# Performance work log

Hardware: AMD Instinct MI355X
Metric: run time of the kernel (lower is better)

## Reference

```python
import jax, jax.numpy as jnp
import numpy as np

B, N, IN_DIM, OUT_DIM = 8, 2048, 128, 128
NEG_SLOPE = 0.2

def setup_inputs() -> dict:
    key = jax.random.key(0)
    k1, k2, k3, k4 = jax.random.split(key, 4)
    x = jax.random.normal(k1, (B, N, IN_DIM), dtype=jnp.float32)
    adj = jax.random.randint(k2, (N, N), 0, 2, dtype=jnp.int32)
    # nn.Linear weight init scale ~ 1/sqrt(fan_in)
    W = jax.random.normal(k3, (IN_DIM, OUT_DIM), dtype=jnp.float32) / np.sqrt(IN_DIM)
    a_vec = jax.random.normal(k4, (2 * OUT_DIM,), dtype=jnp.float32) / np.sqrt(2 * OUT_DIM)
    return {"x": x, "adj": adj, "W": W, "a_vec": a_vec}

def reference(x, adj, W, a_vec):
    # h = x @ W : [b, n, d]
    h = jnp.einsum("bni,io->bno", x, W)
    # Algebraic decomposition of a([h_i, h_j]) = a1.h_i + a2.h_j
    a1, a2 = a_vec[:OUT_DIM], a_vec[OUT_DIM:]
    s_i = h @ a1  # [b, n] score contribution from source node i
    s_j = h @ a2  # [b, n] score contribution from target node j
    e = s_i[:, :, None] + s_j[:, None, :]  # [b, n, n]
    e = jnp.where(e >= 0, e, NEG_SLOPE * e)  # leaky_relu(0.2)
    mask = (adj > 0)[None, :, :]  # [1, n, n] broadcast over batch
    e = jnp.where(mask, e, -jnp.inf)
    alpha = jax.nn.softmax(e, axis=-1)  # [b, n, n]
    out = jnp.einsum("bnm,bmd->bnd", alpha, h)  # [b, n, d]
    return out, alpha
```

## Files before the change

### kernel.cpp

```cpp
#include <hip/hip_runtime.h>
#include <hip/hip_bf16.h>
#include <cstdint>
#include <cstddef>

constexpr int Bn = 8;
constexpr int Nn = 2048;
constexpr int Dn = 128;

typedef __bf16 bf16x8 __attribute__((ext_vector_type(8)));
typedef float f32x4 __attribute__((ext_vector_type(4)));

#define AS1 __attribute__((address_space(1)))
#define AS3 __attribute__((address_space(3)))

static __device__ __forceinline__ void gl_lds16(const void* g, void* l) {
  __builtin_amdgcn_global_load_lds((AS1 const void*)g, (AS3 void*)l, 16, 0, 0);
}

__global__ __launch_bounds__(256) void gat_k0(
    const int* __restrict__ adj, unsigned long long* __restrict__ mask64) {
  const int t = threadIdx.x;
  const size_t g = (size_t)blockIdx.x * 256 + t;
  int v = adj[g];
  unsigned long long bal = __ballot(v > 0);
  if ((t & 63) == 0) mask64[g >> 6] = bal;
}

__global__ __launch_bounds__(256) void gat_k1(
    const float* __restrict__ x, const float* __restrict__ W,
    const float* __restrict__ a_vec,
    __bf16* __restrict__ hT, float* __restrict__ s1, float* __restrict__ s2) {
  __shared__ __align__(16) float Wl[64 * 144];
  __shared__ __align__(16) float xL[32 * 132];

  const int t = threadIdx.x;
  const int r0 = blockIdx.x * 32;
  const int b = r0 >> 11;
  const int n0 = r0 & (Nn - 1);
  const int rp = (t >> 4) << 1;
  const int c0 = (t & 15) << 3;
  const int c0p = c0 + ((c0 >> 5) << 2);

  float acc[2][8];
#pragma unroll
  for (int r = 0; r < 2; ++r)
#pragma unroll
    for (int c = 0; c < 8; ++c) acc[r][c] = 0.f;

#pragma unroll
  for (int it = 0; it < 4; ++it) {
    int idx = t + (it << 8);
    int rr = idx >> 5, kc = (idx & 31) << 2;
    *(float4*)(xL + rr * 132 + kc) = *(const float4*)(x + (size_t)(r0 + rr) * Dn + kc);
  }

  for (int ph = 0; ph < 2; ++ph) {
    if (ph) __syncthreads();
#pragma unroll
    for (int it = 0; it < 8; ++it) {
      int idx = t + (it << 8);
      int kk = idx >> 5, c4 = (idx & 31) << 2;
      int dsto = kk * 144 + c4 + ((c4 >> 5) << 2);
      *(float4*)(Wl + dsto) = *(const float4*)(W + (size_t)((ph << 6) + kk) * Dn + c4);
    }
    __syncthreads();
    const float* xrow = xL + rp * 132 + (ph << 6);
    for (int k = 0; k < 64; ++k) {
      float xa0 = xrow[k];
      float xa1 = xrow[132 + k];
      float4 w0 = *(const float4*)(Wl + k * 144 + c0p);
      float4 w1 = *(const float4*)(Wl + k * 144 + c0p + 4);
      float ws[8] = {w0.x, w0.y, w0.z, w0.w, w1.x, w1.y, w1.z, w1.w};
#pragma unroll
      for (int c = 0; c < 8; ++c) {
        acc[0][c] = fmaf(xa0, ws[c], acc[0][c]);
        acc[1][c] = fmaf(xa1, ws[c], acc[1][c]);
      }
    }
  }

  float q1[2] = {0.f, 0.f}, q2[2] = {0.f, 0.f};
#pragma unroll
  for (int c = 0; c < 8; ++c) {
    float a1c = a_vec[c0 + c];
    float a2c = a_vec[Dn + c0 + c];
    q1[0] = fmaf(acc[0][c], a1c, q1[0]);
    q1[1] = fmaf(acc[1][c], a1c, q1[1]);
    q2[0] = fmaf(acc[0][c], a2c, q2[0]);
    q2[1] = fmaf(acc[1][c], a2c, q2[1]);
  }
#pragma unroll
  for (int d = 1; d < 16; d <<= 1) {
    q1[0] += __shfl_xor(q1[0], d);
    q1[1] += __shfl_xor(q1[1], d);
    q2[0] += __shfl_xor(q2[0], d);
    q2[1] += __shfl_xor(q2[1], d);
  }
  if ((t & 15) == 0) {
    s1[b * Nn + n0 + rp] = q1[0];
    s1[b * Nn + n0 + rp + 1] = q1[1];
    s2[b * Nn + n0 + rp] = q2[0];
    s2[b * Nn + n0 + rp + 1] = q2[1];
  }

#pragma unroll
  for (int c = 0; c < 8; ++c) {
    union { __bf16 h[2]; uint32_t u; } pk;
    pk.h[0] = (__bf16)acc[0][c];
    pk.h[1] = (__bf16)acc[1][c];
    *(uint32_t*)(hT + (size_t)(b * Dn + c0 + c) * Nn + n0 + rp) = pk.u;
  }
}

__global__ __launch_bounds__(512) void gat_k2(
    const uint32_t* __restrict__ mask, const __bf16* __restrict__ hT,
    const float* __restrict__ s1, const float* __restrict__ s2,
    float* __restrict__ out, float* __restrict__ alpha) {
  __shared__ __align__(16) float sj[Nn];
  __shared__ float siv[32], invl[32];
  __shared__ __align__(16) __bf16 Pl[2][32 * 72];
  __shared__ __align__(16) __bf16 hl[2][128 * 64];

  const int t = threadIdx.x;
  const int b = blockIdx.x & 7;
  const int i0 = (blockIdx.x >> 3) << 5;
  const int w = t >> 6, lane = t & 63;
  const int ii = t >> 4, sub = t & 15;
  const int lrow = lane >> 3, ccs = lane & 7;
  const __bf16* __restrict__ hTb = hT + (size_t)b * Dn * Nn;

#pragma unroll
  for (int inst = 0; inst < 2; ++inst) {
    int row = (w << 4) + (inst << 3) + lrow;
    gl_lds16(hTb + (size_t)row * Nn + ((ccs ^ lrow) << 3),
             &hl[0][((w << 4) + (inst << 3)) << 6]);
  }

  *(float4*)(sj + (t << 2)) = *(const float4*)(s2 + b * Nn + (t << 2));
  if (t < 32) siv[t] = s1[b * Nn + i0 + t];
  __syncthreads();

  const int i = i0 + ii;
  const uint32_t* __restrict__ mrow = mask + ((size_t)i << 6);
  const float si = siv[ii];

  float l = 0.f;
  const int wofs = sub >> 3;
  const int bsh = (sub & 7) << 2;
  for (int cc = 0; cc < 32; ++cc) {
    int j = (cc << 6) + (sub << 2);
    uint32_t mw = mrow[(cc << 1) + wofs];
    float4 sv = *(const float4*)(sj + j);
    float e;
    e = si + sv.x; e = fmaxf(e, 0.2f * e); l += ((mw >> (bsh + 0)) & 1u) ? __expf(e) : 0.f;
    e = si + sv.y; e = fmaxf(e, 0.2f * e); l += ((mw >> (bsh + 1)) & 1u) ? __expf(e) : 0.f;
    e = si + sv.z; e = fmaxf(e, 0.2f * e); l += ((mw >> (bsh + 2)) & 1u) ? __expf(e) : 0.f;
    e = si + sv.w; e = fmaxf(e, 0.2f * e); l += ((mw >> (bsh + 3)) & 1u) ? __expf(e) : 0.f;
  }
  l += __shfl_xor(l, 1);
  l += __shfl_xor(l, 2);
  l += __shfl_xor(l, 4);
  l += __shfl_xor(l, 8);
  if (sub == 0) invl[ii] = 1.f / l;
  __syncthreads();
  const float il = invl[ii];

  const int iw = (w & 1) << 4;
  const int nd0 = (w >> 1) << 5;
  const int q16 = lane >> 4, m16 = lane & 15;
  f32x4 acc0 = {0.f, 0.f, 0.f, 0.f}, acc1 = {0.f, 0.f, 0.f, 0.f};
  float* __restrict__ arow = alpha + ((size_t)(b * Nn + i) << 11);

  for (int jt = 0; jt < 32; ++jt) {
    const int buf = jt & 1;
    const int j0 = jt << 6;
    {
      int j = j0 + (sub << 2);
      uint32_t mw = mrow[(j0 >> 5) + wofs];
      float4 sv = *(const float4*)(sj + j);
      float e0 = si + sv.x; e0 = fmaxf(e0, 0.2f * e0);
      float e1 = si + sv.y; e1 = fmaxf(e1, 0.2f * e1);
      float e2 = si + sv.z; e2 = fmaxf(e2, 0.2f * e2);
      float e3 = si + sv.w; e3 = fmaxf(e3, 0.2f * e3);
      float a0 = ((mw >> (bsh + 0)) & 1u) ? __expf(e0) * il : 0.f;
      float a1 = ((mw >> (bsh + 1)) & 1u) ? __expf(e1) * il : 0.f;
      float a2 = ((mw >> (bsh + 2)) & 1u) ? __expf(e2) * il : 0.f;
      float a3 = ((mw >> (bsh + 3)) & 1u) ? __expf(e3) * il : 0.f;
      *(float4*)(arow + j) = make_float4(a0, a1, a2, a3);
      union { __bf16 h[4]; uint2 u; } pk;
      pk.h[0] = (__bf16)a0; pk.h[1] = (__bf16)a1;
      pk.h[2] = (__bf16)a2; pk.h[3] = (__bf16)a3;
      *(uint2*)(&Pl[buf][ii * 72 + (sub << 2)]) = pk.u;
    }
    __syncthreads();
    if (jt < 31) {
      int jn = j0 + 64;
#pragma unroll
      for (int inst = 0; inst < 2; ++inst) {
        int row = (w << 4) + (inst << 3) + lrow;
        gl_lds16(hTb + (size_t)row * Nn + jn + ((ccs ^ lrow) << 3),
                 &hl[buf ^ 1][((w << 4) + (inst << 3)) << 6]);
      }
    }
#pragma unroll
    for (int ks = 0; ks < 2; ++ks) {
      bf16x8 af = *(const bf16x8*)(&Pl[buf][(iw + m16) * 72 + (ks << 5) + (q16 << 3)]);
      {
        int d = nd0 + m16;
        int phys = ((ks << 2) + q16) ^ (d & 7);
        bf16x8 bv = *(const bf16x8*)(&hl[buf][(d << 6) + (phys << 3)]);
        acc0 = __builtin_amdgcn_mfma_f32_16x16x32_bf16(af, bv, acc0, 0, 0, 0);
      }
      {
        int d = nd0 + 16 + m16;
        int phys = ((ks << 2) + q16) ^ (d & 7);
        bf16x8 bv = *(const bf16x8*)(&hl[buf][(d << 6) + (phys << 3)]);
        acc1 = __builtin_amdgcn_mfma_f32_16x16x32_bf16(af, bv, acc1, 0, 0, 0);
      }
    }
  }

#pragma unroll
  for (int nb = 0; nb < 2; ++nb) {
    f32x4 a = nb ? acc1 : acc0;
    int d = nd0 + (nb << 4) + m16;
#pragma unroll
    for (int r = 0; r < 4; ++r) {
      int irow = i0 + iw + (q16 << 2) + r;
      out[((size_t)(b * Nn + irow) << 7) + d] = a[r];
    }
  }
}

extern "C" void kernel_launch(void* const* d_in, const int* in_sizes, int n_in,
                              void* d_out, int out_size, void* d_ws, size_t ws_size,
                              hipStream_t stream) {
  const float* x = (const float*)d_in[0];
  const int* adj = (const int*)d_in[1];
  const float* W = (const float*)d_in[2];
  const float* a_vec = (const float*)d_in[3];

  float* out = (float*)d_out;
  float* alpha = out + (size_t)Bn * Nn * Dn;

  char* ws = (char*)d_ws;
  __bf16* hT = (__bf16*)ws;
  float* s1 = (float*)(ws + (size_t)Bn * Dn * Nn * 2);
  float* s2 = s1 + (size_t)Bn * Nn;
  unsigned long long* mask64 = (unsigned long long*)(s2 + (size_t)Bn * Nn);

  gat_k0<<<(Nn * Nn) / 256, 256, 0, stream>>>(adj, mask64);
  gat_k1<<<512, 256, 0, stream>>>(x, W, a_vec, hT, s1, s2);
  gat_k2<<<512, 512, 0, stream>>>((const uint32_t*)mask64, hT, s1, s2, out, alpha);
}
```

Before: 200.9 us.

## Fuse mask packing into projection kernel and factor exp in attention

Merges the adjacency bitmask kernel into the projection kernel, which removes one launch. The attention kernel now precomputes exp(s_j) and exp(0.2*s_j) per column and factors out per-row exponentials, so the inner loops use multiplies and compares instead of per-element exp. Each block now handles 64 rows with four MFMA accumulators per wave, and alpha and out are written with nontemporal stores. The factored form risks overflow or precision loss when exp of large scores is computed separately, and halving the grid to 256 blocks may reduce occupancy.

```diff
diff --git a/kernel.cpp b/kernel.cpp
--- a/kernel.cpp
+++ b/kernel.cpp
@@ -17,19 +17,11 @@
   __builtin_amdgcn_global_load_lds((AS1 const void*)g, (AS3 void*)l, 16, 0, 0);
 }
 
-__global__ __launch_bounds__(256) void gat_k0(
-    const int* __restrict__ adj, unsigned long long* __restrict__ mask64) {
-  const int t = threadIdx.x;
-  const size_t g = (size_t)blockIdx.x * 256 + t;
-  int v = adj[g];
-  unsigned long long bal = __ballot(v > 0);
-  if ((t & 63) == 0) mask64[g >> 6] = bal;
-}
-
 __global__ __launch_bounds__(256) void gat_k1(
     const float* __restrict__ x, const float* __restrict__ W,
-    const float* __restrict__ a_vec,
-    __bf16* __restrict__ hT, float* __restrict__ s1, float* __restrict__ s2) {
+    const float* __restrict__ a_vec, const int* __restrict__ adj,
+    __bf16* __restrict__ hT, float* __restrict__ s1, float* __restrict__ s2,
+    unsigned long long* __restrict__ mask64) {
   __shared__ __align__(16) float Wl[64 * 144];
   __shared__ __align__(16) float xL[32 * 132];
 
@@ -65,6 +57,7 @@
     }
     __syncthreads();
     const float* xrow = xL + rp * 132 + (ph << 6);
+#pragma unroll 4
     for (int k = 0; k < 64; ++k) {
       float xa0 = xrow[k];
       float xa1 = xrow[132 + k];
@@ -110,124 +103,148 @@
     pk.h[1] = (__bf16)acc[1][c];
     *(uint32_t*)(hT + (size_t)(b * Dn + c0 + c) * Nn + n0 + rp) = pk.u;
   }
-}
-
-__global__ __launch_bounds__(512) void gat_k2(
+
+  {
+    const size_t base = (size_t)blockIdx.x * 8192;
+#pragma unroll 4
+    for (int it = 0; it < 32; ++it) {
+      size_t g = base + (it << 8) + t;
+      int v = __builtin_nontemporal_load(adj + g);
+      unsigned long long bal = __ballot(v > 0);
+      if ((t & 63) == 0) mask64[g >> 6] = bal;
+    }
+  }
+}
+
+__global__ __launch_bounds__(512) void gat_k2b(
     const uint32_t* __restrict__ mask, const __bf16* __restrict__ hT,
     const float* __restrict__ s1, const float* __restrict__ s2,
     float* __restrict__ out, float* __restrict__ alpha) {
-  __shared__ __align__(16) float sj[Nn];
-  __shared__ float siv[32], invl[32];
-  __shared__ __align__(16) __bf16 Pl[2][32 * 72];
+  __shared__ __align__(16) float Qs[Nn];
+  __shared__ __align__(16) float Ss[Nn];
+  __shared__ float ivl[64];
+  __shared__ __align__(16) __bf16 Pl[2][64 * 72];
   __shared__ __align__(16) __bf16 hl[2][128 * 64];
 
   const int t = threadIdx.x;
   const int b = blockIdx.x & 7;
-  const int i0 = (blockIdx.x >> 3) << 5;
+  const int i0 = (blockIdx.x >> 3) << 6;
   const int w = t >> 6, lane = t & 63;
-  const int ii = t >> 4, sub = t & 15;
   const int lrow = lane >> 3, ccs = lane & 7;
   const __bf16* __restrict__ hTb = hT + (size_t)b * Dn * Nn;
 
 #pragma unroll
   for (int inst = 0; inst < 2; ++inst) {
-    int row = (w << 4) + (inst << 3) + lrow;
-    gl_lds16(hTb + (size_t)row * Nn + ((ccs ^ lrow) << 3),
+    gl_lds16(hTb + (size_t)((w << 4) + (inst << 3) + lrow) * Nn + ((ccs ^ lrow) << 3),
              &hl[0][((w << 4) + (inst << 3)) << 6]);
   }
 
-  *(float4*)(sj + (t << 2)) = *(const float4*)(s2 + b * Nn + (t << 2));
-  if (t < 32) siv[t] = s1[b * Nn + i0 + t];
+  {
+    float4 sv = *(const float4*)(s2 + b * Nn + (t << 2));
+    float4 q, s;
+    q.x = __expf(sv.x); q.y = __expf(sv.y); q.z = __expf(sv.z); q.w = __expf(sv.w);
+    s.x = __expf(0.2f * sv.x); s.y = __expf(0.2f * sv.y);
+    s.z = __expf(0.2f * sv.z); s.w = __expf(0.2f * sv.w);
+    *(float4*)(Qs + (t << 2)) = q;
+    *(float4*)(Ss + (t << 2)) = s;
+  }
+  const int ii = t >> 3, sub = t & 7;
+  const float si = s1[b * Nn + i0 + ii];
+  const float Ei = __expf(si);
+  const float Gi = __expf(0.2f * si);
+  const float Ti = __expf(-si);
   __syncthreads();
 
-  const int i = i0 + ii;
-  const uint32_t* __restrict__ mrow = mask + ((size_t)i << 6);
-  const float si = siv[ii];
-
-  float l = 0.f;
-  const int wofs = sub >> 3;
-  const int bsh = (sub & 7) << 2;
-  for (int cc = 0; cc < 32; ++cc) {
-    int j = (cc << 6) + (sub << 2);
-    uint32_t mw = mrow[(cc << 1) + wofs];
-    float4 sv = *(const float4*)(sj + j);
-    float e;
-    e = si + sv.x; e = fmaxf(e, 0.2f * e); l += ((mw >> (bsh + 0)) & 1u) ? __expf(e) : 0.f;
-    e = si + sv.y; e = fmaxf(e, 0.2f * e); l += ((mw >> (bsh + 1)) & 1u) ? __expf(e) : 0.f;
-    e = si + sv.z; e = fmaxf(e, 0.2f * e); l += ((mw >> (bsh + 2)) & 1u) ? __expf(e) : 0.f;
-    e = si + sv.w; e = fmaxf(e, 0.2f * e); l += ((mw >> (bsh + 3)) & 1u) ? __expf(e) : 0.f;
-  }
-  l += __shfl_xor(l, 1);
-  l += __shfl_xor(l, 2);
-  l += __shfl_xor(l, 4);
-  l += __shfl_xor(l, 8);
-  if (sub == 0) invl[ii] = 1.f / l;
+  const uint32_t* __restrict__ mrow = mask + ((size_t)(i0 + ii) << 6);
+  float Aq = 0.f, Bs = 0.f;
+  for (int cc = 0; cc < 64; ++cc) {
+    uint32_t mw = mrow[cc] >> (sub << 2);
+    int j = (cc << 5) + (sub << 2);
+    float4 qv = *(const float4*)(Qs + j);
+    float4 sv = *(const float4*)(Ss + j);
+    float qa[4] = {qv.x, qv.y, qv.z, qv.w};
+    float sa[4] = {sv.x, sv.y, sv.z, sv.w};
+#pragma unroll
+    for (int k = 0; k < 4; ++k) {
+      bool on = (mw >> k) & 1u;
+      bool ge = qa[k] >= Ti;
+      Aq += (on && ge) ? qa[k] : 0.f;
+      Bs += (on && !ge) ? sa[k] : 0.f;
+    }
+  }
+  Aq += __shfl_xor(Aq, 1); Bs += __shfl_xor(Bs, 1);
+  Aq += __shfl_xor(Aq, 2); Bs += __shfl_xor(Bs, 2);
+  Aq += __shfl_xor(Aq, 4); Bs += __shfl_xor(Bs, 4);
+  if (sub == 0) ivl[ii] = 1.f / (Ei * Aq + Gi * Bs);
   __syncthreads();
-  const float il = invl[ii];
-
-  const int iw = (w & 1) << 4;
-  const int nd0 = (w >> 1) << 5;
+  const float il = ivl[ii];
+  const float Pi = Ei * il, Ri = Gi * il;
+
+  const int iw16 = (w & 3) << 4;
+  const int dh = (w >> 2) << 6;
   const int q16 = lane >> 4, m16 = lane & 15;
-  f32x4 acc0 = {0.f, 0.f, 0.f, 0.f}, acc1 = {0.f, 0.f, 0.f, 0.f};
-  float* __restrict__ arow = alpha + ((size_t)(b * Nn + i) << 11);
+  f32x4 acc[4];
+#pragma unroll
+  for (int nb = 0; nb < 4; ++nb) acc[nb] = (f32x4){0.f, 0.f, 0.f, 0.f};
+  float* __restrict__ arow = alpha + ((size_t)(b * Nn + i0 + ii) << 11);
 
   for (int jt = 0; jt < 32; ++jt) {
     const int buf = jt & 1;
     const int j0 = jt << 6;
     {
-      int j = j0 + (sub << 2);
-      uint32_t mw = mrow[(j0 >> 5) + wofs];
-      float4 sv = *(const float4*)(sj + j);
-      float e0 = si + sv.x; e0 = fmaxf(e0, 0.2f * e0);
-      float e1 = si + sv.y; e1 = fmaxf(e1, 0.2f * e1);
-      float e2 = si + sv.z; e2 = fmaxf(e2, 0.2f * e2);
-      float e3 = si + sv.w; e3 = fmaxf(e3, 0.2f * e3);
-      float a0 = ((mw >> (bsh + 0)) & 1u) ? __expf(e0) * il : 0.f;
-      float a1 = ((mw >> (bsh + 1)) & 1u) ? __expf(e1) * il : 0.f;
-      float a2 = ((mw >> (bsh + 2)) & 1u) ? __expf(e2) * il : 0.f;
-      float a3 = ((mw >> (bsh + 3)) & 1u) ? __expf(e3) * il : 0.f;
-      *(float4*)(arow + j) = make_float4(a0, a1, a2, a3);
-      union { __bf16 h[4]; uint2 u; } pk;
-      pk.h[0] = (__bf16)a0; pk.h[1] = (__bf16)a1;
-      pk.h[2] = (__bf16)a2; pk.h[3] = (__bf16)a3;
-      *(uint2*)(&Pl[buf][ii * 72 + (sub << 2)]) = pk.u;
+      int j = j0 + (sub << 3);
+      uint32_t m8 = (mrow[(jt << 1) + (sub >> 2)] >> ((sub & 3) << 3)) & 0xffu;
+      float4 q0 = *(const float4*)(Qs + j);
+      float4 q1 = *(const float4*)(Qs + j + 4);
+      float4 s0 = *(const float4*)(Ss + j);
+      float4 s1v = *(const float4*)(Ss + j + 4);
+      float qa[8] = {q0.x, q0.y, q0.z, q0.w, q1.x, q1.y, q1.z, q1.w};
+      float sa[8] = {s0.x, s0.y, s0.z, s0.w, s1v.x, s1v.y, s1v.z, s1v.w};
+      float av[8];
+#pragma unroll
+      for (int k = 0; k < 8; ++k) {
+        bool ge = qa[k] >= Ti;
+        float val = (ge ? Pi : Ri) * (ge ? qa[k] : sa[k]);
+        av[k] = ((m8 >> k) & 1u) ? val : 0.f;
+      }
+      f32x4 o0 = {av[0], av[1], av[2], av[3]};
+      f32x4 o1 = {av[4], av[5], av[6], av[7]};
+      __builtin_nontemporal_store(o0, (f32x4*)(arow + j));
+      __builtin_nontemporal_store(o1, (f32x4*)(arow + j + 4));
+      union { __bf16 h[8]; uint4 u; } pk;
+#pragma unroll
+      for (int k = 0; k < 8; ++k) pk.h[k] = (__bf16)av[k];
+      *(uint4*)(&Pl[buf][ii * 72 + (sub << 3)]) = pk.u;
     }
     __syncthreads();
     if (jt < 31) {
       int jn = j0 + 64;
 #pragma unroll
       for (int inst = 0; inst < 2; ++inst) {
-        int row = (w << 4) + (inst << 3) + lrow;
-        gl_lds16(hTb + (size_t)row * Nn + jn + ((ccs ^ lrow) << 3),
+        gl_lds16(hTb + (size_t)((w << 4) + (inst << 3) + lrow) * Nn + jn + ((ccs ^ lrow) << 3),
                  &hl[buf ^ 1][((w << 4) + (inst << 3)) << 6]);
       }
     }
 #pragma unroll
     for (int ks = 0; ks < 2; ++ks) {
-      bf16x8 af = *(const bf16x8*)(&Pl[buf][(iw + m16) * 72 + (ks << 5) + (q16 << 3)]);
-      {
-        int d = nd0 + m16;
+      bf16x8 af = *(const bf16x8*)(&Pl[buf][(iw16 + m16) * 72 + (ks << 5) + (q16 << 3)]);
+#pragma unroll
+      for (int nb = 0; nb < 4; ++nb) {
+        int d = dh + (nb << 4) + m16;
         int phys = ((ks << 2) + q16) ^ (d & 7);
         bf16x8 bv = *(const bf16x8*)(&hl[buf][(d << 6) + (phys << 3)]);
-        acc0 = __builtin_amdgcn_mfma_f32_16x16x32_bf16(af, bv, acc0, 0, 0, 0);
-      }
-      {
-        int d = nd0 + 16 + m16;
-        int phys = ((ks << 2) + q16) ^ (d & 7);
-        bf16x8 bv = *(const bf16x8*)(&hl[buf][(d << 6) + (phys << 3)]);
-        acc1 = __builtin_amdgcn_mfma_f32_16x16x32_bf16(af, bv, acc1, 0, 0, 0);
-      }
-    }
-  }
-
-#pragma unroll
-  for (int nb = 0; nb < 2; ++nb) {
-    f32x4 a = nb ? acc1 : acc0;
-    int d = nd0 + (nb << 4) + m16;
+        acc[nb] = __builtin_amdgcn_mfma_f32_16x16x32_bf16(af, bv, acc[nb], 0, 0, 0);
+      }
+    }
+  }
+
+#pragma unroll
+  for (int nb = 0; nb < 4; ++nb) {
+    int d = dh + (nb << 4) + m16;
 #pragma unroll
     for (int r = 0; r < 4; ++r) {
-      int irow = i0 + iw + (q16 << 2) + r;
-      out[((size_t)(b * Nn + irow) << 7) + d] = a[r];
+      int irow = i0 + iw16 + (q16 << 2) + r;
+      __builtin_nontemporal_store(acc[nb][r], out + ((size_t)(b * Nn + irow) << 7) + d);
     }
   }
 }
@@ -249,7 +266,6 @@
   float* s2 = s1 + (size_t)Bn * Nn;
   unsigned long long* mask64 = (unsigned long long*)(s2 + (size_t)Bn * Nn);
 
-  gat_k0<<<(Nn * Nn) / 256, 256, 0, stream>>>(adj, mask64);
-  gat_k1<<<512, 256, 0, stream>>>(x, W, a_vec, hT, s1, s2);
-  gat_k2<<<512, 512, 0, stream>>>((const uint32_t*)mask64, hT, s1, s2, out, alpha);
-}
+  gat_k1<<<512, 256, 0, stream>>>(x, W, a_vec, adj, hT, s1, s2, mask64);
+  gat_k2b<<<256, 512, 0, stream>>>((const uint32_t*)mask64, hT, s1, s2, out, alpha);
+}
```

Result: slower. 215.0 us (+7.0%).
